# Kernel optimization log

Hardware: AMD Instinct MI355X
Metric: run time of the kernel (lower is better)

Reference implementation:

```python
import jax, jax.numpy as jnp
import numpy as np

N_NODES = 50000; N_EDGES = 600000; N_GRAPHS = 128
IN_CH = 128; PROJ = 128; OUT_CH = 128; K = 3; NCLASS = 2; EPS = 1e-5


def _mask():
    # xhi_layer_mask: block i (rows i*OUT_CH:(i+1)*OUT_CH) sees first PROJ*(i+1) input cols
    blocks = []
    for i in range(K):
        m = np.zeros((OUT_CH, PROJ * K), np.float32)
        m[:, :PROJ * (i + 1)] = 1.0
        blocks.append(m)
    return jnp.asarray(np.concatenate(blocks, 0))


def _bn(x, g, b):
    # BatchNorm1d in training mode: biased batch stats, affine g/b
    m = jnp.mean(x, axis=0)
    v = jnp.var(x, axis=0)
    return (x - m) * jax.lax.rsqrt(v + EPS) * g + b


def setup_inputs() -> dict:
    key = jax.random.key(0)
    ks = jax.random.split(key, 10)
    M = OUT_CH * K
    def w(k, shape):
        return jax.random.normal(k, shape, jnp.float32) * 0.05
    return {
        "x": jax.random.normal(ks[0], (N_NODES, IN_CH), jnp.float32),
        "edge_index": jax.random.randint(ks[1], (2, N_EDGES), 0, N_NODES),
        "batch": jnp.sort(jax.random.randint(ks[2], (N_NODES,), 0, N_GRAPHS)),
        "n_graphs": N_GRAPHS,
        "w_rel": w(ks[3], (PROJ, IN_CH)), "b_rel": jnp.zeros((PROJ,), jnp.float32),
        "w_root": w(ks[4], (PROJ, IN_CH)),
        "norm0_g": jnp.ones((PROJ,), jnp.float32), "norm0_b": jnp.zeros((PROJ,), jnp.float32),
        "lin_w": w(ks[5], (M, PROJ * K)), "lin_b": jnp.zeros((M,), jnp.float32),
        "bnh_g": jnp.ones((M,), jnp.float32), "bnh_b": jnp.zeros((M,), jnp.float32),
        "bno_g": jnp.ones((3 * M,), jnp.float32), "bno_b": jnp.zeros((3 * M,), jnp.float32),
        "w1": w(ks[6], (2 * M, 3 * M)), "b1": jnp.zeros((2 * M,), jnp.float32),
        "w2": w(ks[7], (M, 2 * M)), "b2": jnp.zeros((M,), jnp.float32),
        "w3": w(ks[8], (NCLASS, M)), "b3": jnp.zeros((NCLASS,), jnp.float32),
    }


def reference(x, edge_index, batch, n_graphs, w_rel, b_rel, w_root, norm0_g, norm0_b,
              lin_w, lin_b, bnh_g, bnh_b, bno_g, bno_b, w1, b1, w2, b2, w3, b3):
    row, col = edge_index[0], edge_index[1]
    # GraphConv: lin_rel(sum_{j->i} x_j) + lin_root(x_i)
    neigh = jax.ops.segment_sum(x[row], col, num_segments=N_NODES)
    X = neigh @ w_rel.T + b_rel + x @ w_root.T
    X = _bn(X, norm0_g, norm0_b)
    # k-hop polynomial diffusion: A^i X computed as iterative SpMM over edges
    # (A[r,c] = 1 for edge (r,c): (A v)[r] = sum over edges of v[c])
    H = [X]
    cur = X
    for _ in range(K - 1):
        cur = jax.ops.segment_sum(cur[col], row, num_segments=N_NODES)
        H.append(cur)
    Hc = jnp.concatenate(H, axis=1)  # [N, PROJ*K]
    Hm = _bn(Hc @ (lin_w * _mask()).T + lin_b, bnh_g, bnh_b)  # [N, OUT_CH*K]
    # global mean / add / max pooling per graph
    ones = jnp.ones((N_NODES,), jnp.float32)
    cnt = jax.ops.segment_sum(ones, batch, num_segments=n_graphs)
    Hadd = jax.ops.segment_sum(Hm, batch, num_segments=n_graphs)
    Havg = Hadd / jnp.maximum(cnt, 1.0)[:, None]
    Hmax = jax.ops.segment_max(Hm, batch, num_segments=n_graphs)
    Hmax = jnp.where(jnp.isfinite(Hmax), Hmax, 0.0)  # guard empty segments
    Hcat = jnp.concatenate([Havg, Hadd, Hmax], axis=1)  # [G, 3*OUT_CH*K]
    # funnel readout (dropout = identity in eval)
    h = _bn(Hcat, bno_g, bno_b)
    h = jax.nn.relu(h @ w1.T + b1)
    h = jax.nn.relu(h @ w2.T + b2)
    return jax.nn.log_softmax(h @ w3.T + b3, axis=1)
```

## Files before the change

### kernel.cpp

```cpp
#include <hip/hip_runtime.h>
#include <math.h>

#define N_NODES 50000
#define N_EDGES 600000
#define N_GRAPHS 128
#define IN_CH 128
#define PROJ 128
#define OUT_CH 128
#define M_DIM 384
#define HC_DIM 384
#define CAT_DIM 1152
#define H1_DIM 768
#define EPS 1e-5f
#define SCAN_BLK 256
#define NPART 8
#define PART_NODES 6250
#define NPB 64
#define NROWB 391

using bf16x8 = __attribute__((ext_vector_type(8))) short;
using f32x4  = __attribute__((ext_vector_type(4))) float;

__device__ inline unsigned short f2bf(float f) {
  unsigned u = __float_as_uint(f);
  unsigned r = u + 0x7fffu + ((u >> 16) & 1u);
  return (unsigned short)(r >> 16);
}
__device__ inline float bf2f(unsigned h) {
  return __uint_as_float(h << 16);
}

__device__ inline void atomicMaxF(float* addr, float val) {
  int iv = __float_as_int(val);
  if (iv >= 0) atomicMax((int*)addr, iv);
  else         atomicMin((unsigned int*)addr, (unsigned int)iv);
}
__device__ inline void atomicMinF(float* addr, float val) {
  int iv = __float_as_int(val);
  if (iv >= 0) atomicMin((int*)addr, iv);
  else         atomicMax((unsigned int*)addr, (unsigned int)iv);
}

__device__ inline void gld16(const void* g, void* l) {
  __builtin_amdgcn_global_load_lds(
      (const __attribute__((address_space(1))) void*)g,
      (__attribute__((address_space(3))) void*)l, 16, 0, 0);
}

__global__ void init_kernel(const int* __restrict__ batch, float* __restrict__ gmax,
                            float* __restrict__ gmin, int* __restrict__ start) {
  int i = blockIdx.x * blockDim.x + threadIdx.x;
  if (i < N_GRAPHS * M_DIM) {
    gmax[i] = -__builtin_inff();
    gmin[i] =  __builtin_inff();
  }
  if (i < N_NODES) {
    int b = batch[i];
    int bp = (i == 0) ? -1 : batch[i - 1];
    for (int g = bp + 1; g <= b; ++g) start[g] = i;
    if (i == N_NODES - 1)
      for (int g = b + 1; g <= N_GRAPHS; ++g) start[g] = N_NODES;
  }
}

__global__ void cnt_from_bounds_kernel(const int* __restrict__ start, float* __restrict__ cnt) {
  int g = threadIdx.x;
  if (g < N_GRAPHS) cnt[g] = (float)(start[g + 1] - start[g]);
}

__global__ __launch_bounds__(256) void hist_part_kernel(
    const int* __restrict__ row, const int* __restrict__ col,
    int* __restrict__ degA, int* __restrict__ degB) {
  const int part = blockIdx.x & (NPART - 1);
  const int slice = blockIdx.x >> 3;
  const int lo = part * PART_NODES, hi = lo + PART_NODES;
  for (int e = slice * 256 + threadIdx.x; e < N_EDGES; e += NPB * 256) {
    int r = row[e], c = col[e];
    if (c >= lo && c < hi) atomicAdd(&degA[c], 1);
    if (r >= lo && r < hi) atomicAdd(&degB[r], 1);
  }
}

__global__ __launch_bounds__(256) void fill_csr_part_kernel(
    const int* __restrict__ row, const int* __restrict__ col,
    int* __restrict__ cursA, int* __restrict__ eidxA,
    int* __restrict__ cursB, int* __restrict__ eidxB) {
  const int part = blockIdx.x & (NPART - 1);
  const int slice = blockIdx.x >> 3;
  const int lo = part * PART_NODES, hi = lo + PART_NODES;
  for (int e = slice * 256 + threadIdx.x; e < N_EDGES; e += NPB * 256) {
    int r = row[e], c = col[e];
    if (c >= lo && c < hi) eidxA[atomicAdd(&cursA[c], 1)] = r;
    if (r >= lo && r < hi) eidxB[atomicAdd(&cursB[r], 1)] = c;
  }
}

__global__ void scan1_kernel(const int* __restrict__ degA, const int* __restrict__ degB,
                             int* __restrict__ offsA, int* __restrict__ offsB,
                             int* __restrict__ bsumA, int* __restrict__ bsumB, int n) {
  __shared__ int sh[SCAN_BLK];
  const int* deg = blockIdx.y ? degB : degA;
  int* offs = blockIdx.y ? offsB : offsA;
  int* bsum = blockIdx.y ? bsumB : bsumA;
  int i = blockIdx.x * SCAN_BLK + threadIdx.x;
  int v = (i < n) ? deg[i] : 0;
  sh[threadIdx.x] = v; __syncthreads();
  #pragma unroll
  for (int d = 1; d < SCAN_BLK; d <<= 1) {
    int t = (threadIdx.x >= d) ? sh[threadIdx.x - d] : 0;
    __syncthreads();
    sh[threadIdx.x] += t;
    __syncthreads();
  }
  if (i < n) offs[i] = sh[threadIdx.x] - v;
  if (threadIdx.x == SCAN_BLK - 1) bsum[blockIdx.x] = sh[threadIdx.x];
}

__global__ void scan2_kernel(int* __restrict__ bsumA, int* __restrict__ bsumB, int nb) {
  __shared__ int sh[SCAN_BLK];
  int* bsum = blockIdx.y ? bsumB : bsumA;
  int v = (threadIdx.x < nb) ? bsum[threadIdx.x] : 0;
  sh[threadIdx.x] = v; __syncthreads();
  #pragma unroll
  for (int d = 1; d < SCAN_BLK; d <<= 1) {
    int t = (threadIdx.x >= d) ? sh[threadIdx.x - d] : 0;
    __syncthreads();
    sh[threadIdx.x] += t;
    __syncthreads();
  }
  if (threadIdx.x < nb) bsum[threadIdx.x] = sh[threadIdx.x] - v;
}

__global__ void scan3_kernel(int* __restrict__ offsA, int* __restrict__ offsB,
                             const int* __restrict__ bsumA, const int* __restrict__ bsumB,
                             int* __restrict__ cursA, int* __restrict__ cursB, int n) {
  int* offs = blockIdx.y ? offsB : offsA;
  const int* bsum = blockIdx.y ? bsumB : bsumA;
  int* cursor = blockIdx.y ? cursB : cursA;
  int i = blockIdx.x * SCAN_BLK + threadIdx.x;
  if (i < n) {
    int o = offs[i] + bsum[blockIdx.x];
    offs[i] = o;
    cursor[i] = o;
  }
}

__global__ void convert_x_kernel(const float* __restrict__ x, unsigned short* __restrict__ xnb) {
  int t = blockIdx.x * blockDim.x + threadIdx.x;
  if (t >= N_NODES * 32) return;
  int node = t >> 5;
  int c4 = (t & 31) << 2;
  float4 v = *(const float4*)(x + (size_t)node * IN_CH + c4);
  ushort4 h = {f2bf(v.x), f2bf(v.y), f2bf(v.z), f2bf(v.w)};
  *(ushort4*)(xnb + (size_t)node * 256 + 128 + c4) = h;
}

__global__ void convert_wcat_kernel(const float* __restrict__ w_rel, const float* __restrict__ w_root,
                                    unsigned short* __restrict__ wcatb) {
  int t = blockIdx.x * blockDim.x + threadIdx.x;
  if (t >= 128 * 64) return;
  int n = t >> 6;
  int c4 = (t & 63) << 2;
  const float* src = (c4 < 128) ? (w_rel + (size_t)n * 128 + c4)
                                : (w_root + (size_t)n * 128 + (c4 - 128));
  float4 v = *(const float4*)src;
  ushort4 h = {f2bf(v.x), f2bf(v.y), f2bf(v.z), f2bf(v.w)};
  *(ushort4*)(wcatb + (size_t)n * 256 + c4) = h;
}

__global__ void convert_linw_kernel(const float* __restrict__ lin_w, const float* __restrict__ bn_s,
                                    unsigned short* __restrict__ linwb) {
  int t = blockIdx.x * blockDim.x + threadIdx.x;
  if (t >= 384 * 96) return;
  int n = t / 96;
  int c4 = (t - n * 96) << 2;
  float4 v = *(const float4*)(lin_w + (size_t)n * HC_DIM + c4);
  if (c4 < 128) {
    v.x *= bn_s[c4 + 0]; v.y *= bn_s[c4 + 1]; v.z *= bn_s[c4 + 2]; v.w *= bn_s[c4 + 3];
  }
  ushort4 h = {f2bf(v.x), f2bf(v.y), f2bf(v.z), f2bf(v.w)};
  *(ushort4*)(linwb + (size_t)n * HC_DIM + c4) = h;
}

__global__ void linb_fold_kernel(const float* __restrict__ lin_w, const float* __restrict__ lin_b,
                                 const float* __restrict__ bn_t, float* __restrict__ lin_b2) {
  int o = blockIdx.x * blockDim.x + threadIdx.x;
  if (o >= M_DIM) return;
  float s = lin_b[o];
  for (int c = 0; c < 128; ++c) s += bn_t[c] * lin_w[(size_t)o * HC_DIM + c];
  lin_b2[o] = s;
}

__device__ inline void addbf8(float* a, uint4 v) {
  a[0] += bf2f(v.x & 0xffffu); a[1] += bf2f(v.x >> 16);
  a[2] += bf2f(v.y & 0xffffu); a[3] += bf2f(v.y >> 16);
  a[4] += bf2f(v.z & 0xffffu); a[5] += bf2f(v.z >> 16);
  a[6] += bf2f(v.w & 0xffffu); a[7] += bf2f(v.w >> 16);
}

__device__ inline void gather_body(const unsigned short* __restrict__ src,
                                   const int* __restrict__ eidx, int j, int end,
                                   int src_ld, int c, float* a) {
  for (; j + 3 < end; j += 4) {
    int s0 = eidx[j], s1 = eidx[j + 1], s2 = eidx[j + 2], s3 = eidx[j + 3];
    uint4 v0 = *(const uint4*)(src + (size_t)s0 * src_ld + c);
    uint4 v1 = *(const uint4*)(src + (size_t)s1 * src_ld + c);
    uint4 v2 = *(const uint4*)(src + (size_t)s2 * src_ld + c);
    uint4 v3 = *(const uint4*)(src + (size_t)s3 * src_ld + c);
    addbf8(a, v0); addbf8(a, v1); addbf8(a, v2); addbf8(a, v3);
  }
  for (; j < end; ++j) {
    uint4 v0 = *(const uint4*)(src + (size_t)eidx[j] * src_ld + c);
    addbf8(a, v0);
  }
}

__device__ inline void store_bf8(unsigned short* dst, const float* a) {
  uint4 o;
  o.x = (unsigned)f2bf(a[0]) | ((unsigned)f2bf(a[1]) << 16);
  o.y = (unsigned)f2bf(a[2]) | ((unsigned)f2bf(a[3]) << 16);
  o.z = (unsigned)f2bf(a[4]) | ((unsigned)f2bf(a[5]) << 16);
  o.w = (unsigned)f2bf(a[6]) | ((unsigned)f2bf(a[7]) << 16);
  *(uint4*)dst = o;
}

__global__ __launch_bounds__(256) void gather_bf16_kernel(
    const unsigned short* __restrict__ src, const int* __restrict__ offs,
    const int* __restrict__ ends, const int* __restrict__ eidx,
    unsigned short* __restrict__ dst, int src_ld, int dst_ld) {
  int tid = blockIdx.x * blockDim.x + threadIdx.x;
  int node = tid >> 4;
  int c = (tid & 15) << 3;
  if (node >= N_NODES) return;
  float a[8] = {0.f, 0.f, 0.f, 0.f, 0.f, 0.f, 0.f, 0.f};
  gather_body(src, eidx, offs[node], ends[node], src_ld, c, a);
  store_bf8(dst + (size_t)node * dst_ld + c, a);
}

__global__ __launch_bounds__(256) void gather_bn_kernel(
    const unsigned short* __restrict__ src, const int* __restrict__ offs,
    const int* __restrict__ ends, const int* __restrict__ eidx,
    const float* __restrict__ bn_s, const float* __restrict__ bn_t,
    unsigned short* __restrict__ dst, int src_ld, int dst_ld) {
  int tid = blockIdx.x * blockDim.x + threadIdx.x;
  int node = tid >> 4;
  int c = (tid & 15) << 3;
  if (node >= N_NODES) return;
  int j0 = offs[node], end = ends[node];
  float a[8] = {0.f, 0.f, 0.f, 0.f, 0.f, 0.f, 0.f, 0.f};
  gather_body(src, eidx, j0, end, src_ld, c, a);
  float deg = (float)(end - j0);
  #pragma unroll
  for (int k = 0; k < 8; ++k) a[k] = bn_s[c + k] * a[k] + deg * bn_t[c + k];
  store_bf8(dst + (size_t)node * dst_ld + c, a);
}

__device__ inline void stage_async(const unsigned short* __restrict__ src, int src_ld,
                                   int row0, int k0, char* __restrict__ zone, int t) {
  #pragma unroll
  for (int p = 0; p < 4; ++p) {
    int idx = p * 256 + t;
    int r = idx >> 3;
    int slot = idx & 7;
    int sslot = slot ^ (r & 7);
    const char* g = (const char*)(src + (size_t)(row0 + r) * src_ld + k0) + (sslot << 4);
    void* l = zone + p * 4096 + (t >> 6) * 1024;
    gld16(g, l);
  }
}

__device__ inline bf16x8 frag_ld(const char* __restrict__ zone, int row, int slot) {
  return *(const bf16x8*)(zone + row * 128 + ((slot ^ (row & 7)) << 4));
}

__global__ __launch_bounds__(256) void gemm_conv_mfma(
    const unsigned short* __restrict__ xnb, const unsigned short* __restrict__ wcatb,
    const float* __restrict__ b_rel, unsigned short* __restrict__ Hcb,
    float* __restrict__ colsum8, float* __restrict__ colsq8) {
  __shared__ char smem[65536];
  const int bm = blockIdx.x * 128;
  const int t = threadIdx.x;
  const int l = t & 63;
  const int wid = t >> 6;
  const int wr = wid >> 1, wc = wid & 1;
  const int lrow = l & 15, lk = l >> 4;
  f32x4 acc[4][4];
  #pragma unroll
  for (int i = 0; i < 4; ++i)
    #pragma unroll
    for (int jn = 0; jn < 4; ++jn) acc[i][jn] = (f32x4){0.f, 0.f, 0.f, 0.f};
  stage_async(xnb, 256, bm, 0, smem, t);
  stage_async(wcatb, 256, 0, 0, smem + 16384, t);
  __syncthreads();
  int cur = 0;
  for (int st = 0; st < 4; ++st) {
    if (st < 3) {
      char* nz = smem + (cur ^ 1) * 32768;
      stage_async(xnb, 256, bm, (st + 1) * 64, nz, t);
      stage_async(wcatb, 256, 0, (st + 1) * 64, nz + 16384, t);
    }
    const char* zA = smem + cur * 32768;
    const char* zB = zA + 16384;
    #pragma unroll
    for (int kk = 0; kk < 2; ++kk) {
      bf16x8 af[4], bfr[4];
      #pragma unroll
      for (int mf = 0; mf < 4; ++mf) af[mf] = frag_ld(zA, wr * 64 + mf * 16 + lrow, kk * 4 + lk);
      #pragma unroll
      for (int nf = 0; nf < 4; ++nf) bfr[nf] = frag_ld(zB, wc * 64 + nf * 16 + lrow, kk * 4 + lk);
      #pragma unroll
      for (int mf = 0; mf < 4; ++mf)
        #pragma unroll
        for (int nf = 0; nf < 4; ++nf)
          acc[mf][nf] = __builtin_amdgcn_mfma_f32_16x16x32_bf16(af[mf], bfr[nf], acc[mf][nf], 0, 0, 0);
    }
    __syncthreads();
    cur ^= 1;
  }
  float brv[4];
  #pragma unroll
  for (int nf = 0; nf < 4; ++nf) brv[nf] = b_rel[wc * 64 + nf * 16 + lrow];
  #pragma unroll
  for (int mf = 0; mf < 4; ++mf) {
    #pragma unroll
    for (int q = 0; q < 4; ++q) {
      int r = bm + wr * 64 + mf * 16 + lk * 4 + q;
      if (r < N_NODES) {
        #pragma unroll
        for (int nf = 0; nf < 4; ++nf)
          Hcb[(size_t)r * HC_DIM + wc * 64 + nf * 16 + lrow] = f2bf(acc[mf][nf][q] + brv[nf]);
      }
    }
  }
  __syncthreads();
  float* csum = (float*)smem;
  float* csq  = (float*)(smem + 512);
  if (t < 128) { csum[t] = 0.f; csq[t] = 0.f; }
  __syncthreads();
  #pragma unroll
  for (int nf = 0; nf < 4; ++nf) {
    int ccol = wc * 64 + nf * 16 + lrow;
    float s = 0.f, q = 0.f;
    #pragma unroll
    for (int mf = 0; mf < 4; ++mf)
      #pragma unroll
      for (int qq = 0; qq < 4; ++qq) {
        int r = bm + wr * 64 + mf * 16 + lk * 4 + qq;
        if (r < N_NODES) { float v = acc[mf][nf][qq] + brv[nf]; s += v; q += v * v; }
      }
    atomicAdd(&csum[ccol], s);
    atomicAdd(&csq[ccol], q);
  }
  __syncthreads();
  if (t < 128) {
    int cpy = (blockIdx.x & 7) * 128;
    atomicAdd(&colsum8[cpy + t], csum[t]);
    atomicAdd(&colsq8[cpy + t], csq[t]);
  }
}

__global__ void bn_prep_kernel(const float* __restrict__ colsum8, const float* __restrict__ colsq8,
                               const float* __restrict__ g_, const float* __restrict__ b_,
                               float* __restrict__ bn_s, float* __restrict__ bn_t) {
  int c = threadIdx.x;
  float s1 = 0.f, s2 = 0.f;
  #pragma unroll
  for (int k = 0; k < 8; ++k) { s1 += colsum8[k * 128 + c]; s2 += colsq8[k * 128 + c]; }
  float m = s1 * (1.0f / N_NODES);
  float var = s2 * (1.0f / N_NODES) - m * m;
  float sc = g_[c] * rsqrtf(var + EPS);
  bn_s[c] = sc;
  bn_t[c] = b_[c] - m * sc;
}

__global__ __launch_bounds__(256) void gemm_mask_mfma(
    const unsigned short* __restrict__ Hcb, const unsigned short* __restrict__ linwb,
    const float* __restrict__ lin_b2, const int* __restrict__ batch,
    float* __restrict__ gsum, float* __restrict__ gmax, float* __restrict__ gmin,
    float* __restrict__ colsumsq) {
  __shared__ char smem[65536];
  __shared__ int bsh[128];
  const int bid = blockIdx.x;
  const int ybl = 2 - bid / NROWB;
  const int bm = (bid % NROWB) * 128;
  const int bn = ybl * 128;
  const int nstages = 2 * (ybl + 1);
  const int t = threadIdx.x;
  const int l = t & 63;
  const int wid = t >> 6;
  const int wr = wid >> 1, wc = wid & 1;
  const int lrow = l & 15, lk = l >> 4;
  f32x4 acc[4][4];
  #pragma unroll
  for (int i = 0; i < 4; ++i)
    #pragma unroll
    for (int jn = 0; jn < 4; ++jn) acc[i][jn] = (f32x4){0.f, 0.f, 0.f, 0.f};
  stage_async(Hcb, HC_DIM, bm, 0, smem, t);
  stage_async(linwb, HC_DIM, bn, 0, smem + 16384, t);
  __syncthreads();
  int cur = 0;
  for (int st = 0; st < nstages; ++st) {
    if (st + 1 < nstages) {
      char* nz = smem + (cur ^ 1) * 32768;
      stage_async(Hcb, HC_DIM, bm, (st + 1) * 64, nz, t);
      stage_async(linwb, HC_DIM, bn, (st + 1) * 64, nz + 16384, t);
    }
    const char* zA = smem + cur * 32768;
    const char* zB = zA + 16384;
    #pragma unroll
    for (int kk = 0; kk < 2; ++kk) {
      bf16x8 af[4], bfr[4];
      #pragma unroll
      for (int mf = 0; mf < 4; ++mf) af[mf] = frag_ld(zA, wr * 64 + mf * 16 + lrow, kk * 4 + lk);
      #pragma unroll
      for (int nf = 0; nf < 4; ++nf) bfr[nf] = frag_ld(zB, wc * 64 + nf * 16 + lrow, kk * 4 + lk);
      #pragma unroll
      for (int mf = 0; mf < 4; ++mf)
        #pragma unroll
        for (int nf = 0; nf < 4; ++nf)
          acc[mf][nf] = __builtin_amdgcn_mfma_f32_16x16x32_bf16(af[mf], bfr[nf], acc[mf][nf], 0, 0, 0);
    }
    __syncthreads();
    cur ^= 1;
  }
  float lbv[4];
  #pragma unroll
  for (int nf = 0; nf < 4; ++nf) lbv[nf] = lin_b2[bn + wc * 64 + nf * 16 + lrow];
  if (t < 128) bsh[t] = (bm + t < N_NODES) ? batch[bm + t] : -1;
  float* Y = (float*)smem;
  const int col = t & 127;
  const int gcol = bn + col;
  const int r0 = (t >> 7) * 32;
  float sq = 0.f;
  __syncthreads();
  for (int half = 0; half < 2; ++half) {
    if (wr == half) {
      #pragma unroll
      for (int mf = 0; mf < 4; ++mf)
        #pragma unroll
        for (int q = 0; q < 4; ++q) {
          int rr = mf * 16 + lk * 4 + q;
          #pragma unroll
          for (int nf = 0; nf < 4; ++nf)
            Y[rr * 132 + wc * 64 + nf * 16 + lrow] = acc[mf][nf][q] + lbv[nf];
        }
    }
    __syncthreads();
    int curg = -1;
    float s = 0.f, mx = 0.f, mn = 0.f;
    for (int rr = 0; rr < 32; ++rr) {
      int g = bsh[half * 64 + r0 + rr];
      if (g < 0) break;
      float y = Y[(r0 + rr) * 132 + col];
      sq += y * y;
      if (g != curg) {
        if (curg >= 0) {
          atomicAdd(&gsum[curg * M_DIM + gcol], s);
          atomicMaxF(&gmax[curg * M_DIM + gcol], mx);
          atomicMinF(&gmin[curg * M_DIM + gcol], mn);
        }
        curg = g; s = y; mx = y; mn = y;
      } else {
        s += y; mx = fmaxf(mx, y); mn = fminf(mn, y);
      }
    }
    if (curg >= 0) {
      atomicAdd(&gsum[curg * M_DIM + gcol], s);
      atomicMaxF(&gmax[curg * M_DIM + gcol], mx);
      atomicMinF(&gmin[curg * M_DIM + gcol], mn);
    }
    __syncthreads();
  }
  atomicAdd(&colsumsq[gcol], sq);
}

__device__ inline float block_sum128(float v, float* red) {
  int t = threadIdx.x;
  red[t] = v; __syncthreads();
  #pragma unroll
  for (int s = 64; s >= 1; s >>= 1) {
    if (t < s) red[t] += red[t + s];
    __syncthreads();
  }
  float r = red[0];
  __syncthreads();
  return r;
}

__device__ inline void bn_write_col(float v, int col, const float* __restrict__ bg,
                                    const float* __restrict__ bb, float* __restrict__ h0T,
                                    float* red) {
  float s1 = block_sum128(v, red);
  float s2 = block_sum128(v * v, red);
  float m = s1 * (1.0f / N_GRAPHS);
  float var = s2 * (1.0f / N_GRAPHS) - m * m;
  float sc = bg[col] * rsqrtf(var + EPS);
  h0T[(size_t)col * N_GRAPHS + threadIdx.x] = (v - m) * sc + bb[col];
}

__global__ __launch_bounds__(128) void finalize_kernel(
    const float* __restrict__ gsum, const float* __restrict__ gmax,
    const float* __restrict__ gmin, const float* __restrict__ colsumsq,
    const float* __restrict__ cnt, const float* __restrict__ bnh_g,
    const float* __restrict__ bnh_b, const float* __restrict__ bno_g,
    const float* __restrict__ bno_b, float* __restrict__ h0T) {
  __shared__ float red[128];
  int c = blockIdx.x;
  int g = threadIdx.x;
  float vsum = gsum[g * M_DIM + c];
  float colsum = block_sum128(vsum, red);
  float m = colsum * (1.0f / N_NODES);
  float var = colsumsq[c] * (1.0f / N_NODES) - m * m;
  float s = bnh_g[c] * rsqrtf(var + EPS);
  float t = bnh_b[c] - m * s;
  float cg = cnt[g];
  float hadd = s * vsum + cg * t;
  float havg = hadd / fmaxf(cg, 1.0f);
  float hmax = 0.f;
  if (cg > 0.f)
    hmax = (s >= 0.f ? s * gmax[g * M_DIM + c] : s * gmin[g * M_DIM + c]) + t;
  bn_write_col(havg, c,        bno_g, bno_b, h0T, red);
  bn_write_col(hadd, 384 + c,  bno_g, bno_b, h0T, red);
  bn_write_col(hmax, 768 + c,  bno_g, bno_b, h0T, red);
}

__global__ __launch_bounds__(128) void mlp_kernel(
    const float* __restrict__ inT, const float* __restrict__ W,
    const float* __restrict__ bias, float* __restrict__ outT, int Kdim, int do_relu) {
  __shared__ float wrow[CAT_DIM];
  int oc = blockIdx.x;
  int g = threadIdx.x;
  for (int k = g; k < Kdim; k += 128) wrow[k] = W[(size_t)oc * Kdim + k];
  __syncthreads();
  float acc = bias[oc];
  for (int k = 0; k < Kdim; ++k) acc += inT[(size_t)k * N_GRAPHS + g] * wrow[k];
  if (do_relu) acc = fmaxf(acc, 0.f);
  outT[(size_t)oc * N_GRAPHS + g] = acc;
}

__global__ __launch_bounds__(128) void head_kernel(
    const float* __restrict__ h2T, const float* __restrict__ w3,
    const float* __restrict__ b3, float* __restrict__ out) {
  int g = threadIdx.x;
  float z0 = b3[0], z1 = b3[1];
  for (int k = 0; k < M_DIM; ++k) {
    float v = h2T[(size_t)k * N_GRAPHS + g];
    z0 += v * w3[k];
    z1 += v * w3[M_DIM + k];
  }
  float mz = fmaxf(z0, z1);
  float lse = mz + logf(expf(z0 - mz) + expf(z1 - mz));
  out[g * 2 + 0] = z0 - lse;
  out[g * 2 + 1] = z1 - lse;
}

extern "C" void kernel_launch(void* const* d_in, const int* in_sizes, int n_in,
                              void* d_out, int out_size, void* d_ws, size_t ws_size,
                              hipStream_t stream) {
  const float* x       = (const float*)d_in[0];
  const int*   row     = (const int*)d_in[1];
  const int*   col     = row + N_EDGES;
  const int*   batch   = (const int*)d_in[2];
  const float* w_rel   = (const float*)d_in[4];
  const float* b_rel   = (const float*)d_in[5];
  const float* w_root  = (const float*)d_in[6];
  const float* norm0_g = (const float*)d_in[7];
  const float* norm0_b = (const float*)d_in[8];
  const float* lin_w   = (const float*)d_in[9];
  const float* lin_b   = (const float*)d_in[10];
  const float* bnh_g   = (const float*)d_in[11];
  const float* bnh_b   = (const float*)d_in[12];
  const float* bno_g   = (const float*)d_in[13];
  const float* bno_b   = (const float*)d_in[14];
  const float* w1      = (const float*)d_in[15];
  const float* b1      = (const float*)d_in[16];
  const float* w2      = (const float*)d_in[17];
  const float* b2      = (const float*)d_in[18];
  const float* w3      = (const float*)d_in[19];
  const float* b3      = (const float*)d_in[20];
  float* out = (float*)d_out;

  char* ws = (char*)d_ws;
  size_t off = 0;
  auto allocb = [&](size_t nbytes) {
    char* p = ws + off;
    off += ((nbytes + 255) & ~(size_t)255);
    return p;
  };
  int*   degA      = (int*)allocb(N_NODES * 4);
  int*   degB      = (int*)allocb(N_NODES * 4);
  float* gsum      = (float*)allocb((size_t)N_GRAPHS * M_DIM * 4);
  float* colsumsq  = (float*)allocb(M_DIM * 4);
  float* colsum8   = (float*)allocb(8 * PROJ * 4);
  float* colsq8    = (float*)allocb(8 * PROJ * 4);
  size_t zero_bytes = off;
  float* cnt    = (float*)allocb(N_GRAPHS * 4);
  int*   gstart = (int*)allocb((N_GRAPHS + 1) * 4);
  float* bn_s   = (float*)allocb(PROJ * 4);
  float* bn_t   = (float*)allocb(PROJ * 4);
  float* lin_b2 = (float*)allocb(M_DIM * 4);
  int*   offsA = (int*)allocb(N_NODES * 4);
  int*   cursA = (int*)allocb(N_NODES * 4);
  int*   offsB = (int*)allocb(N_NODES * 4);
  int*   cursB = (int*)allocb(N_NODES * 4);
  int*   bsumA = (int*)allocb(SCAN_BLK * 4);
  int*   bsumB = (int*)allocb(SCAN_BLK * 4);
  int*   eidxA = (int*)allocb(N_EDGES * 4);
  int*   eidxB = (int*)allocb(N_EDGES * 4);
  unsigned short* Hcb   = (unsigned short*)allocb((size_t)N_NODES * HC_DIM * 2);
  unsigned short* xnb   = (unsigned short*)allocb((size_t)N_NODES * 256 * 2);
  unsigned short* wcatb = (unsigned short*)allocb(128 * 256 * 2);
  unsigned short* linwb = (unsigned short*)allocb(384 * 384 * 2);
  float* gmax  = (float*)allocb((size_t)N_GRAPHS * M_DIM * 4);
  float* gmin  = (float*)allocb((size_t)N_GRAPHS * M_DIM * 4);
  float* h0T   = (float*)allocb((size_t)CAT_DIM * N_GRAPHS * 4);
  float* h1T   = (float*)allocb((size_t)H1_DIM * N_GRAPHS * 4);
  float* h2T   = (float*)allocb((size_t)M_DIM * N_GRAPHS * 4);

  const int NB = (N_NODES + SCAN_BLK - 1) / SCAN_BLK;

  hipMemsetAsync(d_ws, 0, zero_bytes, stream);
  init_kernel<<<(N_NODES + 255) / 256, 256, 0, stream>>>(batch, gmax, gmin, gstart);
  cnt_from_bounds_kernel<<<1, 128, 0, stream>>>(gstart, cnt);

  hist_part_kernel<<<NPART * NPB, 256, 0, stream>>>(row, col, degA, degB);
  scan1_kernel<<<dim3(NB, 2), SCAN_BLK, 0, stream>>>(degA, degB, offsA, offsB, bsumA, bsumB, N_NODES);
  scan2_kernel<<<dim3(1, 2), SCAN_BLK, 0, stream>>>(bsumA, bsumB, NB);
  scan3_kernel<<<dim3(NB, 2), SCAN_BLK, 0, stream>>>(offsA, offsB, bsumA, bsumB, cursA, cursB, N_NODES);
  fill_csr_part_kernel<<<NPART * NPB, 256, 0, stream>>>(row, col, cursA, eidxA, cursB, eidxB);

  convert_x_kernel<<<(N_NODES * 32 + 255) / 256, 256, 0, stream>>>(x, xnb);
  convert_wcat_kernel<<<(128 * 64 + 255) / 256, 256, 0, stream>>>(w_rel, w_root, wcatb);

  gather_bf16_kernel<<<(N_NODES * 16 + 255) / 256, 256, 0, stream>>>(
      xnb + 128, offsA, cursA, eidxA, xnb, 256, 256);
  gemm_conv_mfma<<<NROWB, 256, 0, stream>>>(xnb, wcatb, b_rel, Hcb, colsum8, colsq8);
  bn_prep_kernel<<<1, 128, 0, stream>>>(colsum8, colsq8, norm0_g, norm0_b, bn_s, bn_t);
  convert_linw_kernel<<<(384 * 96 + 255) / 256, 256, 0, stream>>>(lin_w, bn_s, linwb);
  linb_fold_kernel<<<3, 128, 0, stream>>>(lin_w, lin_b, bn_t, lin_b2);
  gather_bn_kernel<<<(N_NODES * 16 + 255) / 256, 256, 0, stream>>>(
      Hcb, offsB, cursB, eidxB, bn_s, bn_t, Hcb + 128, HC_DIM, HC_DIM);
  gather_bf16_kernel<<<(N_NODES * 16 + 255) / 256, 256, 0, stream>>>(
      Hcb + 128, offsB, cursB, eidxB, Hcb + 256, HC_DIM, HC_DIM);
  gemm_mask_mfma<<<NROWB * 3, 256, 0, stream>>>(
      Hcb, linwb, lin_b2, batch, gsum, gmax, gmin, colsumsq);
  finalize_kernel<<<M_DIM, 128, 0, stream>>>(gsum, gmax, gmin, colsumsq, cnt,
                                             bnh_g, bnh_b, bno_g, bno_b, h0T);
  mlp_kernel<<<H1_DIM, 128, 0, stream>>>(h0T, w1, b1, h1T, CAT_DIM, 1);
  mlp_kernel<<<M_DIM, 128, 0, stream>>>(h1T, w2, b2, h2T, H1_DIM, 1);
  head_kernel<<<1, 128, 0, stream>>>(h2T, w3, b3, out);
}
```

Measured before the change: 400.0 us.

## Drop LDS double buffering in both MFMA GEMMs to raise occupancy

Both bf16 MFMA GEMM kernels (the GraphConv projection and the masked lin GEMM) go from ping-pong LDS buffers to a single-buffer scheme. Each K-stage is now loaded synchronously between two barriers. This halves the shared memory per block from 64 KB to about 32 KB, so more blocks can be resident per CU and hide memory latency through extra waves. The cost is that the in-block overlap of the next tile's load with the current tile's MFMA work is gone, and there is one extra barrier per stage.

```diff
diff --git a/kernel.cpp b/kernel.cpp
--- a/kernel.cpp
+++ b/kernel.cpp
@@ -277,7 +277,9 @@
     const unsigned short* __restrict__ xnb, const unsigned short* __restrict__ wcatb,
     const float* __restrict__ b_rel, unsigned short* __restrict__ Hcb,
     float* __restrict__ colsum8, float* __restrict__ colsq8) {
-  __shared__ char smem[65536];
+  __shared__ char smem[32768];
+  char* zoneA = smem;
+  char* zoneB = smem + 16384;
   const int bm = blockIdx.x * 128;
   const int t = threadIdx.x;
   const int l = t & 63;
@@ -289,33 +291,24 @@
   for (int i = 0; i < 4; ++i)
     #pragma unroll
     for (int jn = 0; jn < 4; ++jn) acc[i][jn] = (f32x4){0.f, 0.f, 0.f, 0.f};
-  stage_async(xnb, 256, bm, 0, smem, t);
-  stage_async(wcatb, 256, 0, 0, smem + 16384, t);
-  __syncthreads();
-  int cur = 0;
   for (int st = 0; st < 4; ++st) {
-    if (st < 3) {
-      char* nz = smem + (cur ^ 1) * 32768;
-      stage_async(xnb, 256, bm, (st + 1) * 64, nz, t);
-      stage_async(wcatb, 256, 0, (st + 1) * 64, nz + 16384, t);
-    }
-    const char* zA = smem + cur * 32768;
-    const char* zB = zA + 16384;
+    __syncthreads();
+    stage_async(xnb, 256, bm, st * 64, zoneA, t);
+    stage_async(wcatb, 256, 0, st * 64, zoneB, t);
+    __syncthreads();
     #pragma unroll
     for (int kk = 0; kk < 2; ++kk) {
       bf16x8 af[4], bfr[4];
       #pragma unroll
-      for (int mf = 0; mf < 4; ++mf) af[mf] = frag_ld(zA, wr * 64 + mf * 16 + lrow, kk * 4 + lk);
-      #pragma unroll
-      for (int nf = 0; nf < 4; ++nf) bfr[nf] = frag_ld(zB, wc * 64 + nf * 16 + lrow, kk * 4 + lk);
+      for (int mf = 0; mf < 4; ++mf) af[mf] = frag_ld(zoneA, wr * 64 + mf * 16 + lrow, kk * 4 + lk);
+      #pragma unroll
+      for (int nf = 0; nf < 4; ++nf) bfr[nf] = frag_ld(zoneB, wc * 64 + nf * 16 + lrow, kk * 4 + lk);
       #pragma unroll
       for (int mf = 0; mf < 4; ++mf)
         #pragma unroll
         for (int nf = 0; nf < 4; ++nf)
           acc[mf][nf] = __builtin_amdgcn_mfma_f32_16x16x32_bf16(af[mf], bfr[nf], acc[mf][nf], 0, 0, 0);
     }
-    __syncthreads();
-    cur ^= 1;
   }
   float brv[4];
   #pragma unroll
@@ -378,8 +371,10 @@
     const float* __restrict__ lin_b2, const int* __restrict__ batch,
     float* __restrict__ gsum, float* __restrict__ gmax, float* __restrict__ gmin,
     float* __restrict__ colsumsq) {
-  __shared__ char smem[65536];
+  __shared__ char smem[33792];
   __shared__ int bsh[128];
+  char* zoneA = smem;
+  char* zoneB = smem + 16384;
   const int bid = blockIdx.x;
   const int ybl = 2 - bid / NROWB;
   const int bm = (bid % NROWB) * 128;
@@ -395,33 +390,24 @@
   for (int i = 0; i < 4; ++i)
     #pragma unroll
     for (int jn = 0; jn < 4; ++jn) acc[i][jn] = (f32x4){0.f, 0.f, 0.f, 0.f};
-  stage_async(Hcb, HC_DIM, bm, 0, smem, t);
-  stage_async(linwb, HC_DIM, bn, 0, smem + 16384, t);
-  __syncthreads();
-  int cur = 0;
   for (int st = 0; st < nstages; ++st) {
-    if (st + 1 < nstages) {
-      char* nz = smem + (cur ^ 1) * 32768;
-      stage_async(Hcb, HC_DIM, bm, (st + 1) * 64, nz, t);
-      stage_async(linwb, HC_DIM, bn, (st + 1) * 64, nz + 16384, t);
-    }
-    const char* zA = smem + cur * 32768;
-    const char* zB = zA + 16384;
+    __syncthreads();
+    stage_async(Hcb, HC_DIM, bm, st * 64, zoneA, t);
+    stage_async(linwb, HC_DIM, bn, st * 64, zoneB, t);
+    __syncthreads();
     #pragma unroll
     for (int kk = 0; kk < 2; ++kk) {
       bf16x8 af[4], bfr[4];
       #pragma unroll
-      for (int mf = 0; mf < 4; ++mf) af[mf] = frag_ld(zA, wr * 64 + mf * 16 + lrow, kk * 4 + lk);
-      #pragma unroll
-      for (int nf = 0; nf < 4; ++nf) bfr[nf] = frag_ld(zB, wc * 64 + nf * 16 + lrow, kk * 4 + lk);
+      for (int mf = 0; mf < 4; ++mf) af[mf] = frag_ld(zoneA, wr * 64 + mf * 16 + lrow, kk * 4 + lk);
+      #pragma unroll
+      for (int nf = 0; nf < 4; ++nf) bfr[nf] = frag_ld(zoneB, wc * 64 + nf * 16 + lrow, kk * 4 + lk);
       #pragma unroll
       for (int mf = 0; mf < 4; ++mf)
         #pragma unroll
         for (int nf = 0; nf < 4; ++nf)
           acc[mf][nf] = __builtin_amdgcn_mfma_f32_16x16x32_bf16(af[mf], bfr[nf], acc[mf][nf], 0, 0, 0);
     }
-    __syncthreads();
-    cur ^= 1;
   }
   float lbv[4];
   #pragma unroll
```

After: 393.0 us (median of 2 runs). No clear change (-1.8%).
